# Optimization experiments

Hardware: AMD Instinct MI355X
Metric: run time of the kernel (lower is better)

Reference implementation:

```python
import jax, jax.numpy as jnp
import numpy as np

B, N_PTS, N_IN = 1, 29696, 1024
E1, E2, E3, NZ = 512, 512, 2048, 32
D1, D2, D3 = 2048, 512, 512
K = 100
V_DOF = 1.0      # Student-t dof `v`
C_CONST = 1.0    # args.c
EPS = 1e-5


def setup_inputs() -> dict:
    key = jax.random.key(0)
    ks = jax.random.split(key, 24)

    def lin_w(k, din, dout):
        return (jax.random.normal(k, (din, dout), jnp.float32) / np.float32(np.sqrt(din)))

    return {
        "x": jax.random.normal(ks[0], (B, N_PTS, N_IN), jnp.float32),
        "t1_coordinate": jax.random.normal(ks[1], (B, N_PTS, 3), jnp.float32),
        "cluster_layer": jax.random.normal(ks[2], (B, K, NZ), jnp.float32),
        "We1": lin_w(ks[3], N_IN, E1), "be1": jnp.zeros((E1,), jnp.float32),
        "We2": lin_w(ks[4], E1, E2),   "be2": jnp.zeros((E2,), jnp.float32),
        "We3": lin_w(ks[5], E2, E3),   "be3": jnp.zeros((E3,), jnp.float32),
        "Wz":  lin_w(ks[6], E3, NZ),   "bz":  jnp.zeros((NZ,), jnp.float32),
        "Wd1": lin_w(ks[7], NZ, D1),   "bd1": jnp.zeros((D1,), jnp.float32),
        "Wd2": lin_w(ks[8], D1, D2),   "bd2": jnp.zeros((D2,), jnp.float32),
        "Wd3": lin_w(ks[9], D2, D3),   "bd3": jnp.zeros((D3,), jnp.float32),
        "Wxb": lin_w(ks[10], D3, N_IN), "bxb": jnp.zeros((N_IN,), jnp.float32),
    }


def _std(a, axis=-1, keepdims=True):
    # torch.std default is unbiased (ddof=1)
    return jnp.std(a, axis=axis, keepdims=keepdims, ddof=1)


def reference(x, t1_coordinate, cluster_layer,
              We1, be1, We2, be2, We3, be3, Wz, bz,
              Wd1, bd1, Wd2, bd2, Wd3, bd3, Wxb, bxb):
    relu = jax.nn.relu
    # --- AE encode / decode ---
    h = relu(x @ We1 + be1)
    h = relu(h @ We2 + be2)
    h = relu(h @ We3 + be3)
    z = h @ Wz + bz                                   # [B, N, NZ]
    d = relu(z @ Wd1 + bd1)
    d = relu(d @ Wd2 + bd2)
    d = relu(d @ Wd3 + bd3)
    x_bar = d @ Wxb + bxb                             # [B, N, N_IN]

    # --- positional modulation + per-point normalization ---
    t1 = t1_coordinate / 100.0
    cos_mult = jnp.prod(t1, axis=-1, keepdims=True) * 0.99 + 1.0   # [B, N, 1]
    zp = z * cos_mult                                 # with_pos=True
    zp = (zp - zp.mean(axis=-1, keepdims=True)) / _std(zp)

    # --- distance to cluster centers + (inverted) Student-t assignment ---
    # [B, N, K]
    dist = jnp.sum((zp[:, :, None, :] - cluster_layer[:, None, :, :]) ** 2, axis=-1)
    q = 1.0 / (EPS + dist / V_DOF)
    q = q ** (-(V_DOF + 1.0) / 2.0)
    q = q / jnp.sum(q, axis=-1, keepdims=True)
    predict = jnp.argmax(q, axis=-1)                  # [B, N] int

    # --- stat_target_distribution (batch_size == 1 path) ---
    index = q.shape[1]                                # N_PTS
    u = q.sum(axis=1, keepdims=True)                  # [B, 1, K]
    u = (u - u.mean(axis=-1, keepdims=True)) / _std(u)

    cnt = jnp.zeros((B, K), jnp.int32).at[jnp.arange(B)[:, None], predict].add(1)
    Ncnt = jnp.where(cnt > 0, cnt, 1).astype(q.dtype)  # torch.ones init for empty clusters

    temp_q = (1.0 - q) ** 2 * jnp.log(q) * index      # [B, N, K], negative
    # v_i = sum over flat(N*K) of sqrt(-N_i / temp_q) = sqrt(N_i) * S
    S = jnp.sum(jnp.sqrt(-1.0 / temp_q), axis=(1, 2))  # [B]
    v_vec = jnp.sqrt(Ncnt) * S[:, None]               # [B, K]
    v_vec = v_vec[:, None, :]                         # [B, 1, K]
    v_vec = (v_vec - v_vec.mean(axis=-1, keepdims=True)) / _std(v_vec)
    v_vec = jax.lax.stop_gradient(v_vec)              # computed under no_grad in torch

    # batch_size == 1: global min shift
    u = u - u.min() + 0.001
    v_vec = v_vec - v_vec.min() + 0.001

    f = u + v_vec + C_CONST                           # [B, 1, K]
    w1 = q ** 2 / f
    p0 = w1 / w1.sum(axis=-1, keepdims=True)
    # first step: self.p = p, then self.p = 0.1*p + 0.9*self.p.detach()
    p = 0.1 * p0 + 0.9 * jax.lax.stop_gradient(p0)

    # --- losses ---
    kl_loss = jnp.mean(p * (jnp.log(p) - jnp.log(q))) * 0.01
    re_loss = jnp.mean((x_bar - x) ** 2)
    D = jnp.sum((cluster_layer[:, :, None, :] - cluster_layer[:, None, :, :]) ** 2, axis=-1)
    mean_distance = D.sum() / (D.size - D.shape[0] * D.shape[1])
    u_loss = (1.0 / mean_distance) * 0.01
    loss = kl_loss + re_loss + u_loss
    return predict, loss
```

## Files before the change

### kernel.cpp

```cpp
#include <hip/hip_runtime.h>
#include <math.h>

#define M_PTS 29696
#define KCL 100
#define NZ_DIM 32
#define ASTR 256

typedef _Float16 h8 __attribute__((ext_vector_type(8)));
typedef _Float16 h4 __attribute__((ext_vector_type(4)));
typedef float f4 __attribute__((ext_vector_type(4)));

__device__ __forceinline__ void load_lds16(const void* g, void* l) {
    __builtin_amdgcn_global_load_lds(
        (const __attribute__((address_space(1))) void*)g,
        (__attribute__((address_space(3))) void*)l, 16, 0, 0);
}

struct PrepW {
    const float* W[8];
    _Float16* Th[8];
    _Float16* Tl[8];
    int K[8];
    int N[8];
    int off[9];
};

__global__ __launch_bounds__(256)
void prep_weights(PrepW a, float* __restrict__ Zf, float* __restrict__ US,
                  int* __restrict__ CS, int* __restrict__ CTRS,
                  double* __restrict__ DBL)
{
    __shared__ float t[32][33];
    const int bid = blockIdx.x;
    const int tid = threadIdx.x;

    if (bid < (M_PTS*NZ_DIM/4/256)) {
        const size_t zi = ((size_t)bid*256 + tid)*4;
        *(float4*)(Zf + zi) = make_float4(0.0f, 0.0f, 0.0f, 0.0f);
    }
    if (bid == 0) {
        if (tid < KCL) { US[tid*ASTR] = 0.0f; CS[tid*ASTR] = 0; }
        if (tid == KCL) { CTRS[0] = 0; CTRS[1] = 0; }
        if (tid < 8) DBL[tid] = 0.0;
    }

    int w = 0;
    #pragma unroll
    for (int i = 1; i < 8; ++i) w += (bid >= a.off[i]);
    const int local = bid - a.off[w];
    const int K = a.K[w], N = a.N[w];
    const int tx = N >> 5;
    const int sh = __builtin_ctz(tx);
    const int n0 = (local & (tx - 1)) * 32, k0 = (local >> sh) * 32;
    const float* W = a.W[w];
    _Float16* WTh = a.Th[w];
    _Float16* WTl = a.Tl[w];

    {
        int r = tid / 8, c = (tid % 8) * 4;
        const float4 v = *(const float4*)(W + (size_t)(k0 + r) * N + n0 + c);
        t[r][c+0] = v.x; t[r][c+1] = v.y; t[r][c+2] = v.z; t[r][c+3] = v.w;
    }
    __syncthreads();
    {
        int r = tid / 8, c = (tid % 8) * 4;
        h4 hi, lo;
        #pragma unroll
        for (int u = 0; u < 4; ++u) {
            float f = t[c+u][r];
            _Float16 h = (_Float16)f;
            hi[u] = h; lo[u] = (_Float16)(f - (float)h);
        }
        *(h4*)(WTh + (size_t)(n0 + r) * K + k0 + c) = hi;
        *(h4*)(WTl + (size_t)(n0 + r) * K + k0 + c) = lo;
    }
}

template<int WM,int WN,int TM,int TN,bool RELU,int MODE,int TERMS,int ASRC=0>
__global__ __launch_bounds__(WM*WN*64)
void gemm_sp(const _Float16* __restrict__ Ahp, const _Float16* __restrict__ Alp,
             const _Float16* __restrict__ Bhp, const _Float16* __restrict__ Blp,
             const float* __restrict__ bias,
             _Float16* __restrict__ Ch, _Float16* __restrict__ Cl,
             float* __restrict__ Cf, const float* __restrict__ Xref,
             double* __restrict__ loss_acc,
             int M, int N, int K)
{
    constexpr int BM = WM*TM*16, BN = WN*TN*16, NW = WM*WN;
    constexpr int PL = (TERMS == 3) ? 2 : 1;
    constexpr int CA = BM/16, CB = BN/16;
    constexpr int STRIDE = PL*(BM+BN)*32;
    constexpr int NPW = ((MODE == 5) ? 1 : (CA/NW)*PL)
                      + ((CB >= NW) ? (CB/NW) : 1)*PL;
    constexpr int NPW_B = ((CB >= NW) ? (CB/NW) : 1)*PL;
    static_assert(ASRC == 0 || (TERMS == 3 && (CA/NW) == 2 && MODE == 0),
                  "ASRC=1 path sized for the L1 config");
    constexpr int EXTRA = (MODE == 5) ? (2048 + 4096) : 0;
    __shared__ __align__(16) _Float16 smem[2*STRIDE + EXTRA];

    const int tid = threadIdx.x;
    const int wave = tid >> 6, lane = tid & 63;
    const int wm = wave / WN, wn = wave % WN;
    const int lrow = lane & 15, lq = lane >> 4;
    const int sw = (lrow >> 1) & 3;
    const int lr4 = lane >> 2, lc4 = lane & 3;
    const int bm0 = blockIdx.y * BM, bn0 = blockIdx.x * BN;

    f4 acc[TM][TN];
    #pragma unroll
    for (int i = 0; i < TM; ++i)
        #pragma unroll
        for (int j = 0; j < TN; ++j)
            acc[i][j] = (f4)0.0f;

    auto stage = [&](int s, int k0) {
        _Float16* base = smem + s*STRIDE;
        if constexpr (MODE == 5) {
            int r_in = lane >> 2;
            int gk = (lane & 3) ^ ((r_in >> 1) & 3);
            load_lds16(Alp + (size_t)(k0 + wn*16 + r_in)*32 + gk*8,
                       smem + 2*STRIDE + s*1024 + wn*512);
        } else if constexpr (ASRC == 1) {
        } else {
            #pragma unroll
            for (int c = wave; c < CA; c += NW) {
                int r = c*16 + lr4;
                int g = lc4 ^ ((r >> 1) & 3);
                size_t goff = (size_t)(bm0 + r)*K + k0 + g*8;
                load_lds16(Ahp + goff, base + c*512);
                if (PL == 2) load_lds16(Alp + goff, base + BM*32 + c*512);
            }
        }
        if (CB >= NW) {
            #pragma unroll
            for (int c = wave; c < CB; c += NW) {
                int r = c*16 + lr4;
                int g = lc4 ^ ((r >> 1) & 3);
                size_t goff = (size_t)(bn0 + r)*K + k0 + g*8;
                load_lds16(Bhp + goff, base + PL*BM*32 + c*512);
                if (PL == 2) load_lds16(Blp + goff, base + PL*BM*32 + BN*32 + c*512);
            }
        } else {
            int c = wave % CB;
            int r = c*16 + lr4;
            int g = lc4 ^ ((r >> 1) & 3);
            size_t goff = (size_t)(bn0 + r)*K + k0 + g*8;
            load_lds16(Bhp + goff, base + PL*BM*32 + c*512);
            if (PL == 2) load_lds16(Blp + goff, base + PL*BM*32 + BN*32 + c*512);
        }
    };

    auto stageA_load = [&](int k0, float4 (&ar)[4]) {
        if constexpr (ASRC == 1) {
            #pragma unroll
            for (int u = 0; u < 2; ++u) {
                int c = wave + u*NW;
                int r = c*16 + lr4;
                int g = lc4 ^ ((r >> 1) & 3);
                const float* src = Xref + (size_t)(bm0 + r)*K + k0 + g*8;
                ar[u*2+0] = *(const float4*)(src);
                ar[u*2+1] = *(const float4*)(src + 4);
            }
        }
    };
    auto stageA_write = [&](int s, const float4 (&ar)[4]) {
        if constexpr (ASRC == 1) {
            _Float16* base = smem + s*STRIDE;
            #pragma unroll
            for (int u = 0; u < 2; ++u) {
                int c = wave + u*NW;
                float fv[8] = {ar[u*2].x, ar[u*2].y, ar[u*2].z, ar[u*2].w,
                               ar[u*2+1].x, ar[u*2+1].y, ar[u*2+1].z, ar[u*2+1].w};
                h8 hi, lo;
                #pragma unroll
                for (int q = 0; q < 8; ++q) {
                    _Float16 h = (_Float16)fv[q];
                    hi[q] = h; lo[q] = (_Float16)(fv[q] - (float)h);
                }
                *(h8*)(base + c*512 + lane*8) = hi;
                *(h8*)(base + BM*32 + c*512 + lane*8) = lo;
            }
        }
    };

    h8 zfr[(MODE == 5) ? TM : 1];
    auto computeA = [&](int ds, int s) {
        if constexpr (MODE == 5) {
            const _Float16* wslot = smem + 2*STRIDE + ds*1024 + wn*512;
            const float* bds = (const float*)(smem + 2*STRIDE + 2048);
            h8 wf = *(const h8*)(wslot + lrow*32 + ((lq ^ sw)*8));
            float bv = bds[s*32 + wn*16 + lrow];
            _Float16* areg = smem + ds*STRIDE;
            const int kc = wn*16 + lrow;
            #pragma unroll
            for (int i2 = 0; i2 < TM; ++i2) {
                f4 cc = __builtin_amdgcn_mfma_f32_16x16x32_f16(zfr[i2], wf, (f4)0.0f, 0, 0, 0);
                int cch = wm*TM + i2;
                #pragma unroll
                for (int r = 0; r < 4; ++r) {
                    float v = fmaxf(cc[r] + bv, 0.0f);
                    int r16 = lq*4 + r;
                    areg[cch*512 + r16*32 + (((kc >> 3) ^ ((r16 >> 1) & 3))*8) + (kc & 7)]
                        = (_Float16)v;
                }
            }
        }
    };

    float4 ar0[4];
    if constexpr (ASRC == 1) stageA_load(0, ar0);
    if constexpr (MODE == 5) {
        #pragma unroll
        for (int c = wave; c < 8; c += NW)
            load_lds16(Xref + c*256 + lane*4, smem + 2*STRIDE + 2048 + c*512);
        const float* zf32 = (const float*)Ahp;
        const float* bz32 = (const float*)Cl;
        float4 b0 = *(const float4*)(bz32 + lq*8);
        float4 b1 = *(const float4*)(bz32 + lq*8 + 4);
        float bb[8] = {b0.x,b0.y,b0.z,b0.w,b1.x,b1.y,b1.z,b1.w};
        #pragma unroll
        for (int i2 = 0; i2 < TM; ++i2) {
            const float* zsrc = zf32 + (size_t)(bm0 + (wm*TM + i2)*16 + lrow)*32 + lq*8;
            float4 z0 = *(const float4*)(zsrc);
            float4 z1 = *(const float4*)(zsrc + 4);
            float zz[8] = {z0.x,z0.y,z0.z,z0.w,z1.x,z1.y,z1.z,z1.w};
            #pragma unroll
            for (int q = 0; q < 8; ++q) zfr[i2][q] = (_Float16)(zz[q] + bb[q]);
        }
    }
    stage(0, 0);
    if constexpr (ASRC == 1) {
        __builtin_amdgcn_s_waitcnt(0x0F70 | NPW_B);
        stageA_write(0, ar0);
        asm volatile("s_waitcnt lgkmcnt(0)" ::: "memory");
    }
    if constexpr (MODE == 5) {
        __builtin_amdgcn_s_waitcnt(0x0F70);
        __builtin_amdgcn_s_barrier();
        computeA(0, 0);
        asm volatile("s_waitcnt lgkmcnt(0)" ::: "memory");
        __builtin_amdgcn_s_barrier();
    }

    const int steps = K >> 5;
    for (int i = 0; i < steps; ++i) {
        const int sel = i & 1;
        float4 arn[4];
        if (i + 1 < steps) {
            if constexpr (ASRC == 1) stageA_load((i + 1) << 5, arn);
            stage(sel ^ 1, (i + 1) << 5);
            __builtin_amdgcn_s_waitcnt(0x0F70 | NPW);
        } else {
            __builtin_amdgcn_s_waitcnt(0x0F70);
        }
        __builtin_amdgcn_s_barrier();

        const _Float16* base = smem + sel*STRIDE;
        h8 ah[TM], al[TM], bh[TN], bl[TN];
        #pragma unroll
        for (int i2 = 0; i2 < TM; ++i2) {
            int row = (wm*TM + i2)*16 + lrow;
            int off = row*32 + ((lq ^ sw)*8);
            ah[i2] = *(const h8*)(base + off);
            if (PL == 2) al[i2] = *(const h8*)(base + BM*32 + off);
        }
        #pragma unroll
        for (int j = 0; j < TN; ++j) {
            int row = (wn*TN + j)*16 + lrow;
            int off = row*32 + ((lq ^ sw)*8);
            bh[j] = *(const h8*)(base + PL*BM*32 + off);
            if (PL == 2) bl[j] = *(const h8*)(base + PL*BM*32 + BN*32 + off);
        }
        if constexpr (ASRC == 1) {
            if (i + 1 < steps) {
                __builtin_amdgcn_s_waitcnt(0x0F70 | NPW_B);
                stageA_write(sel ^ 1, arn);
            }
        }
        if constexpr (MODE == 5) {
            if (i + 1 < steps) {
                __builtin_amdgcn_s_waitcnt(0x0F70 | (NPW - 1));
                computeA(sel ^ 1, i + 1);
            }
        }
        #pragma unroll
        for (int i2 = 0; i2 < TM; ++i2)
            #pragma unroll
            for (int j = 0; j < TN; ++j)
                acc[i2][j] = __builtin_amdgcn_mfma_f32_16x16x32_f16(ah[i2], bh[j], acc[i2][j], 0, 0, 0);
        if (TERMS == 3) {
            #pragma unroll
            for (int i2 = 0; i2 < TM; ++i2)
                #pragma unroll
                for (int j = 0; j < TN; ++j)
                    acc[i2][j] = __builtin_amdgcn_mfma_f32_16x16x32_f16(ah[i2], bl[j], acc[i2][j], 0, 0, 0);
            #pragma unroll
            for (int i2 = 0; i2 < TM; ++i2)
                #pragma unroll
                for (int j = 0; j < TN; ++j)
                    acc[i2][j] = __builtin_amdgcn_mfma_f32_16x16x32_f16(al[i2], bh[j], acc[i2][j], 0, 0, 0);
        }
        if constexpr (MODE == 5 || ASRC == 1) {
            asm volatile("s_waitcnt lgkmcnt(0)" ::: "memory");
        }
        __builtin_amdgcn_s_barrier();
    }

    if constexpr (MODE == 4) {
        static_assert(WN*16 == 32, "MODE 4 needs N2=32 across WN waves");
        static_assert(BM*BN <= STRIDE, "MODE 4 tile planes must fit smem");
        constexpr int PLANE = BM*BN;
        constexpr int NC2 = BN/32;
        constexpr int MF2 = TM;
        const _Float16* Wh = (const _Float16*)Ch;
        const _Float16* Wl = (const _Float16*)Cl;
        _Float16* th = smem;
        _Float16* tl = smem + PLANE;

        const int n2 = wn*16 + lrow;
        h8 b2h[NC2], b2l[NC2];
        #pragma unroll
        for (int cc = 0; cc < NC2; ++cc) {
            size_t go = (size_t)n2*N + bn0 + cc*32 + lq*8;
            b2h[cc] = *(const h8*)(Wh + go);
            b2l[cc] = *(const h8*)(Wl + go);
        }

        #pragma unroll
        for (int j = 0; j < TN; ++j) {
            int col = (wn*TN + j)*16 + lrow;
            float bj = bias[bn0 + col];
            int c = col >> 5, kk = col & 31;
            #pragma unroll
            for (int i = 0; i < TM; ++i) {
                int m0 = (wm*TM + i)*16 + lq*4;
                #pragma unroll
                for (int r = 0; r < 4; ++r) {
                    float v = acc[i][j][r] + bj;
                    if (RELU) v = fmaxf(v, 0.0f);
                    int m = m0 + r;
                    int a = c*(BM*32) + m*32 + (((kk >> 3) ^ ((m >> 1) & 3))*8) + (kk & 7);
                    _Float16 hh = (_Float16)v;
                    th[a] = hh;
                    tl[a] = (_Float16)(v - (float)hh);
                }
            }
        }
        __syncthreads();

        f4 acc2[MF2];
        #pragma unroll
        for (int mf = 0; mf < MF2; ++mf) acc2[mf] = (f4)0.0f;
        #pragma unroll
        for (int mf = 0; mf < MF2; ++mf) {
            int mrow = (wm*TM + mf)*16 + lrow;
            #pragma unroll
            for (int cc = 0; cc < NC2; ++cc) {
                int off = cc*(BM*32) + mrow*32 + ((lq ^ sw)*8);
                h8 a2h = *(const h8*)(th + off);
                h8 a2l = *(const h8*)(tl + off);
                acc2[mf] = __builtin_amdgcn_mfma_f32_16x16x32_f16(a2h, b2h[cc], acc2[mf], 0, 0, 0);
                acc2[mf] = __builtin_amdgcn_mfma_f32_16x16x32_f16(a2h, b2l[cc], acc2[mf], 0, 0, 0);
                acc2[mf] = __builtin_amdgcn_mfma_f32_16x16x32_f16(a2l, b2h[cc], acc2[mf], 0, 0, 0);
            }
        }
        #pragma unroll
        for (int mf = 0; mf < MF2; ++mf) {
            int rb = bm0 + (wm*TM + mf)*16 + lq*4;
            #pragma unroll
            for (int r = 0; r < 4; ++r)
                atomicAdd(&Cf[(size_t)(rb + r)*32 + n2], acc2[mf][r]);
        }
        return;
    }

    float lsum = 0.0f;
    #pragma unroll
    for (int j = 0; j < TN; ++j) {
        int col = bn0 + (wn*TN + j)*16 + lrow;
        float bj = bias[col];
        #pragma unroll
        for (int i = 0; i < TM; ++i) {
            int rbase = bm0 + (wm*TM + i)*16 + lq*4;
            #pragma unroll
            for (int r = 0; r < 4; ++r) {
                float v = acc[i][j][r] + bj;
                if (RELU) v = fmaxf(v, 0.0f);
                size_t idx = (size_t)(rbase + r)*N + col;
                if (MODE == 2) {
                    float d = v - Xref[idx];
                    lsum = fmaf(d, d, lsum);
                } else if (MODE == 0) {
                    _Float16 hh = (_Float16)v;
                    __builtin_nontemporal_store(hh, &Ch[idx]);
                    __builtin_nontemporal_store((_Float16)(v - (float)hh), &Cl[idx]);
                } else if (MODE == 1) {
                    _Float16 hh = (_Float16)v;
                    __builtin_nontemporal_store(hh, &Ch[idx]);
                    __builtin_nontemporal_store(v, &Cf[idx]);
                } else {
                    __builtin_nontemporal_store((_Float16)v, &Ch[idx]);
                }
            }
        }
    }
    if (MODE == 2) {
        for (int off = 32; off > 0; off >>= 1) lsum += __shfl_down(lsum, off, 64);
        __syncthreads();
        float* sc = (float*)smem;
        if (lane == 0) sc[wave] = lsum;
        __syncthreads();
        if (tid == 0) {
            double t = 0.0;
            for (int w = 0; w < NW; ++w) t += (double)sc[w];
            atomicAdd(loss_acc, t);
        }
    }
}

__device__ __forceinline__ float blk_sum_f(float v, float* sh) {
    int tid = threadIdx.x;
    sh[tid] = v; __syncthreads();
    for (int s = 128; s > 0; s >>= 1) { if (tid < s) sh[tid] += sh[tid+s]; __syncthreads(); }
    float r = sh[0]; __syncthreads();
    return r;
}
__device__ __forceinline__ float blk_min_f(float v, float* sh) {
    int tid = threadIdx.x;
    sh[tid] = v; __syncthreads();
    for (int s = 128; s > 0; s >>= 1) { if (tid < s) sh[tid] = fminf(sh[tid], sh[tid+s]); __syncthreads(); }
    float r = sh[0]; __syncthreads();
    return r;
}

__global__ __launch_bounds__(256)
void cluster_pass(const float* __restrict__ z, const float* __restrict__ bz,
                  const float* __restrict__ t1,
                  const float* __restrict__ clusters,
                  float* __restrict__ D, float* __restrict__ ROWSUM,
                  float* __restrict__ pred_out, float* __restrict__ u_acc,
                  int* __restrict__ cnt, double* __restrict__ dbl,
                  float* __restrict__ f_out, int* __restrict__ blkctr)
{
    __shared__ __align__(16) float cl[KCL*33];
    __shared__ __align__(16) float Ds[64*KCL];
    __shared__ float u_s[KCL];
    __shared__ int cnt_s[KCL];
    __shared__ float swave[4];
    __shared__ float bzs[NZ_DIM];
    __shared__ int lastFlag;
    const int tid = threadIdx.x;
    const int lane = tid & 63;
    for (int i = tid; i < KCL*NZ_DIM; i += 256) cl[(i >> 5)*33 + (i & 31)] = clusters[i];
    if (tid < KCL) { u_s[tid] = 0.0f; cnt_s[tid] = 0; }
    if (tid < NZ_DIM) bzs[tid] = bz[tid];
    __syncthreads();

    const int p  = (blockIdx.x*256 + tid) >> 2;
    const int pl = tid >> 2;
    const int kg = tid & 3;

    float zr[NZ_DIM];
    const float a = t1[p*3+0]*0.01f, b = t1[p*3+1]*0.01f, c = t1[p*3+2]*0.01f;
    const float cm = a*b*c*0.99f + 1.0f;
    float mean = 0.0f;
    {
        const float4* zv = (const float4*)(z + (size_t)p*NZ_DIM);
        #pragma unroll
        for (int u = 0; u < 8; ++u) {
            float4 v = zv[u];
            zr[u*4+0] = (v.x + bzs[u*4+0])*cm; mean += zr[u*4+0];
            zr[u*4+1] = (v.y + bzs[u*4+1])*cm; mean += zr[u*4+1];
            zr[u*4+2] = (v.z + bzs[u*4+2])*cm; mean += zr[u*4+2];
            zr[u*4+3] = (v.w + bzs[u*4+3])*cm; mean += zr[u*4+3];
        }
    }
    mean *= (1.0f/NZ_DIM);
    float var = 0.0f;
    #pragma unroll
    for (int i = 0; i < NZ_DIM; ++i) { float d = zr[i]-mean; var += d*d; }
    const float istd = 1.0f / sqrtf(var * (1.0f/(NZ_DIM-1)));
    #pragma unroll
    for (int i = 0; i < NZ_DIM; ++i) zr[i] = (zr[i]-mean)*istd;

    float vals[25];
    float rowsum = 0.0f, best = -1.0f; int bk = 0;
    #pragma unroll
    for (int j = 0; j < 25; ++j) {
        const int k = kg + 4*j;
        float d = 0.0f;
        #pragma unroll
        for (int i = 0; i < NZ_DIM; ++i) { float t = zr[i]-cl[k*33+i]; d = fmaf(t,t,d); }
        float val = 1e-5f + d;
        vals[j] = val;
        rowsum += val;
        if (val > best) { best = val; bk = k; }
        Ds[pl*KCL + k] = val;
    }
    rowsum += __shfl_xor(rowsum, 1);
    rowsum += __shfl_xor(rowsum, 2);
    #pragma unroll
    for (int m = 1; m <= 2; m <<= 1) {
        float ov = __shfl_xor(best, m);
        int   ok = __shfl_xor(bk, m);
        if (ov > best || (ov == best && ok < bk)) { best = ov; bk = ok; }
    }
    if (kg == 0) {
        pred_out[p] = (float)bk;
        atomicAdd(&cnt_s[bk], 1);
        ROWSUM[p] = rowsum;
    }

    __syncthreads();
    {
        float4* dst = (float4*)(D + (size_t)blockIdx.x * (64*KCL));
        const float4* src = (const float4*)Ds;
        for (int q = tid; q < (64*KCL)/4; q += 256) dst[q] = src[q];
    }

    const float inv_rs = 1.0f/rowsum;
    float Sp = 0.0f;
    #pragma unroll
    for (int j = 0; j < 25; ++j) {
        float qv = vals[j]*inv_rs;
        float lq = logf(qv);
        float om = 1.0f - qv;
        Sp += sqrtf(-1.0f/(om*om*lq*(float)M_PTS));
        float qs = qv;
        qs += __shfl_xor(qs, 4);
        qs += __shfl_xor(qs, 8);
        qs += __shfl_xor(qs, 16);
        qs += __shfl_xor(qs, 32);
        if (lane < 4) atomicAdd(&u_s[lane + 4*j], qs);
    }
    for (int off = 32; off > 0; off >>= 1) Sp += __shfl_down(Sp, off, 64);
    if (lane == 0) swave[tid >> 6] = Sp;
    __syncthreads();
    if (tid < KCL) {
        atomicAdd(&u_acc[tid*ASTR], u_s[tid]);
        int c2 = cnt_s[tid];
        if (c2) atomicAdd(&cnt[tid*ASTR], c2);
    }
    if (tid == 0) atomicAdd(&dbl[0], (double)(swave[0]+swave[1]+swave[2]+swave[3]));

    __syncthreads();
    if (tid == 0) {
        int old = atomicAdd(blkctr, 1);
        lastFlag = (old == (int)gridDim.x - 1);
    }
    __syncthreads();
    if (!lastFlag) return;

    float* shF = cl;
    double* shD = (double*)&cl[1024];
    const bool act = (tid < KCL);
    const float S = (float)atomicAdd(&dbl[0], 0.0);

    float uv = act ? atomicAdd(&u_acc[tid*ASTR], 0.0f) : 0.0f;
    float um = blk_sum_f(uv, shF) * (1.0f/KCL);
    float ud = act ? (uv - um) : 0.0f;
    float uvar = blk_sum_f(ud*ud, shF) * (1.0f/(KCL-1));
    float un = ud / sqrtf(uvar);
    float umin = blk_min_f(act ? un : 3.0e38f, shF);
    float ufin = un - umin + 0.001f;

    float vv = 0.0f;
    if (act) { int cc2 = atomicAdd(&cnt[tid*ASTR], 0); if (cc2 < 1) cc2 = 1; vv = sqrtf((float)cc2) * S; }
    float vm = blk_sum_f(vv, shF) * (1.0f/KCL);
    float vd = act ? (vv - vm) : 0.0f;
    float vvar = blk_sum_f(vd*vd, shF) * (1.0f/(KCL-1));
    float vn = vd / sqrtf(vvar);
    float vmin = blk_min_f(act ? vn : 3.0e38f, shF);
    float vfin = vn - vmin + 0.001f;

    if (act) f_out[tid] = ufin + vfin + 1.0f;

    double dp = 0.0;
    for (int pair = tid; pair < KCL*KCL; pair += 256) {
        int i = pair / KCL, j = pair % KCL;
        float d = 0.0f;
        #pragma unroll
        for (int t2 = 0; t2 < NZ_DIM; ++t2) {
            float x = clusters[i*NZ_DIM+t2] - clusters[j*NZ_DIM+t2];
            d = fmaf(x, x, d);
        }
        dp += (double)d;
    }
    shD[tid] = dp; __syncthreads();
    for (int s = 128; s > 0; s >>= 1) { if (tid < s) shD[tid] += shD[tid+s]; __syncthreads(); }
    if (tid == 0) {
        dbl[3] = 0.01 * (double)(KCL*KCL - KCL) / shD[0];
    }
}

__global__ __launch_bounds__(256)
void kl_pass(const float* __restrict__ D, const float* __restrict__ ROWSUM,
             const float* __restrict__ f, double* __restrict__ dbl,
             float* __restrict__ out, int* __restrict__ blkctr)
{
    __shared__ __align__(16) float Ds[64*KCL];
    __shared__ float fs[KCL], lfs[KCL];
    __shared__ float swave[4];
    __shared__ int lastFlag;
    const int tid = threadIdx.x;
    const int lane = tid & 63;
    {
        const float4* src = (const float4*)(D + (size_t)blockIdx.x * (64*KCL));
        float4* dst = (float4*)Ds;
        for (int q = tid; q < (64*KCL)/4; q += 256) dst[q] = src[q];
    }
    if (tid < KCL) { float fv = f[tid]; fs[tid] = fv; lfs[tid] = logf(fv); }
    __syncthreads();

    const int p  = (blockIdx.x*256 + tid) >> 2;
    const int pl = tid >> 2;
    const int kg = tid & 3;

    float vals[25];
    #pragma unroll
    for (int j = 0; j < 25; ++j) vals[j] = Ds[pl*KCL + kg + 4*j];

    float sv = 0.0f;
    #pragma unroll
    for (int j = 0; j < 25; ++j) { float v = vals[j]; sv += v*v/fs[kg + 4*j]; }
    sv += __shfl_xor(sv, 1);
    sv += __shfl_xor(sv, 2);

    const float rowsum = ROWSUM[p];
    const float lrs = logf(rowsum), lsv = logf(sv);
    const float inv_sv = 1.0f/sv;
    float klp = 0.0f;
    #pragma unroll
    for (int j = 0; j < 25; ++j) {
        const int k = kg + 4*j;
        float v = vals[j];
        float pv = v*v/fs[k]*inv_sv;
        klp += pv*(logf(v) - lfs[k] - lsv + lrs);
    }
    for (int off = 32; off > 0; off >>= 1) klp += __shfl_down(klp, off, 64);
    if (lane == 0) swave[tid >> 6] = klp;
    __syncthreads();
    if (tid == 0) atomicAdd(&dbl[1], (double)(swave[0]+swave[1]+swave[2]+swave[3]));

    __syncthreads();
    if (tid == 0) {
        int old = atomicAdd(blkctr, 1);
        lastFlag = (old == (int)gridDim.x - 1);
    }
    __syncthreads();
    if (!lastFlag) return;
    if (tid == 0) {
        double kl = atomicAdd(&dbl[1], 0.0) / (double)((size_t)M_PTS*KCL) * 0.01;
        double re = dbl[2] / (double)((size_t)M_PTS*1024);
        out[0] = (float)(kl + re + dbl[3]);
    }
}

extern "C" void kernel_launch(void* const* d_in, const int* in_sizes, int n_in,
                              void* d_out, int out_size, void* d_ws, size_t ws_size,
                              hipStream_t stream)
{
    const float* x   = (const float*)d_in[0];
    const float* t1c = (const float*)d_in[1];
    const float* clu = (const float*)d_in[2];
    const float* We1 = (const float*)d_in[3];  const float* be1 = (const float*)d_in[4];
    const float* We2 = (const float*)d_in[5];  const float* be2 = (const float*)d_in[6];
    const float* We3 = (const float*)d_in[7];  const float* be3 = (const float*)d_in[8];
    const float* Wz  = (const float*)d_in[9];  const float* bz  = (const float*)d_in[10];
    const float* Wd1 = (const float*)d_in[11]; const float* bd1 = (const float*)d_in[12];
    const float* Wd2 = (const float*)d_in[13]; const float* bd2 = (const float*)d_in[14];
    const float* Wd3 = (const float*)d_in[15]; const float* bd3 = (const float*)d_in[16];
    const float* Wxb = (const float*)d_in[17]; const float* bxb = (const float*)d_in[18];
    float* out = (float*)d_out;

    const size_t M = M_PTS;
    _Float16* H = (_Float16*)d_ws;
    size_t o = 0;
    _Float16* BIGh = H + o; o += M*2048;
    _Float16* BIGl = H + o; o += M*2048;
    _Float16* S1h  = H + o; o += M*512;
    _Float16* S1l  = H + o; o += M*512;
    _Float16* S2h  = H + o; o += M*512;
    _Float16* S2l  = H + o; o += M*512;
    _Float16* Zh   = H + o; o += M*32;
    _Float16* Zl   = H + o; o += M*32;
    _Float16* We1h = H + o; o += 512*1024; _Float16* We1l = H + o; o += 512*1024;
    _Float16* We2h = H + o; o += 512*512;  _Float16* We2l = H + o; o += 512*512;
    _Float16* We3h = H + o; o += 2048*512; _Float16* We3l = H + o; o += 2048*512;
    _Float16* Wzh  = H + o; o += 32*2048;  _Float16* Wzl  = H + o; o += 32*2048;
    _Float16* Wd1h = H + o; o += 2048*32;  _Float16* Wd1l = H + o; o += 2048*32;
    _Float16* Wd2h = H + o; o += 512*2048; _Float16* Wd2l = H + o; o += 512*2048;
    _Float16* Wd3h = H + o; o += 512*512;  _Float16* Wd3l = H + o; o += 512*512;
    _Float16* Wxbh = H + o; o += 1024*512; _Float16* Wxbl = H + o; o += 1024*512;
    float* fpr = (float*)(H + o);
    float* Zf  = fpr;        fpr += M*32;
    float* US  = fpr;        fpr += KCL*ASTR;
    int*   CS  = (int*)fpr;  fpr += KCL*ASTR;
    float* F   = fpr;        fpr += 128;
    int*   CTRS = (int*)fpr; fpr += 16;
    double* DBL = (double*)(((uintptr_t)fpr + 15) & ~(uintptr_t)15);

    float* Dm  = (float*)S1l;
    float* RSm = (float*)S2l;

    {
        PrepW pa;
        const float* Ws[8]  = {We1, We2, We3, Wz, Wd1, Wd2, Wd3, Wxb};
        _Float16* Ths[8]    = {We1h, We2h, We3h, Wzh, Wd1h, Wd2h, Wd3h, Wxbh};
        _Float16* Tls[8]    = {We1l, We2l, We3l, Wzl, Wd1l, Wd2l, Wd3l, Wxbl};
        const int Ks[8]     = {1024, 512, 512, 2048, 32, 2048, 512, 512};
        const int Ns[8]     = {512, 512, 2048, 32, 2048, 512, 512, 1024};
        int acc = 0;
        for (int i = 0; i < 8; ++i) {
            pa.W[i] = Ws[i]; pa.Th[i] = Ths[i]; pa.Tl[i] = Tls[i];
            pa.K[i] = Ks[i]; pa.N[i] = Ns[i];
            pa.off[i] = acc;
            acc += (Ns[i] >> 5) * (Ks[i] >> 5);
        }
        pa.off[8] = acc;
        prep_weights<<<acc, 256, 0, stream>>>(pa, Zf, US, CS, CTRS, DBL);
    }

    const int MB = M_PTS/128;
    gemm_sp<2,2,4,4,true ,0,3,1><<<dim3(4,  MB), 256, 0, stream>>>(nullptr, nullptr, We1h, We1l, be1, S1h, S1l, nullptr, x, nullptr, M, 512,  1024);
    gemm_sp<2,2,4,4,true ,0,3><<<dim3(4,  MB), 256, 0, stream>>>(S1h, S1l, We2h, We2l, be2, S2h, S2l, nullptr, nullptr, nullptr, M, 512,  512);
    gemm_sp<2,2,4,4,true ,4,3><<<dim3(16, MB), 256, 0, stream>>>(S2h, S2l, We3h, We3l, be3, Wzh, Wzl, Zf, nullptr, nullptr, M, 2048, 512);
    gemm_sp<2,2,4,4,true ,5,1><<<dim3(4,  MB), 256, 0, stream>>>((const _Float16*)Zf, Wd1h, Wd2h, nullptr, bd2, S1h, (_Float16*)bz, nullptr, bd1, nullptr, M, 512,  2048);
    gemm_sp<2,2,4,4,true ,3,1><<<dim3(4,  MB), 256, 0, stream>>>(S1h, nullptr, Wd3h, nullptr, bd3, S2h,  nullptr, nullptr, nullptr, nullptr, M, 512,  512);
    gemm_sp<2,2,4,4,false,2,1><<<dim3(8,  MB), 256, 0, stream>>>(S2h, nullptr, Wxbh, nullptr, bxb, nullptr, nullptr, nullptr, x, DBL+2, M, 1024, 512);

    const int PB = (M_PTS*4)/256;
    cluster_pass<<<PB, 256, 0, stream>>>(Zf, bz, t1c, clu, Dm, RSm, out, US, CS, DBL, F, &CTRS[0]);
    kl_pass<<<PB, 256, 0, stream>>>(Dm, RSm, F, DBL, out + M_PTS, &CTRS[1]);
}
```

Baseline: 937.1 us.

## Fuse cluster and KL passes with grid-wide spin barrier, keep distances in registers

Merges the cluster-assignment and KL-loss kernels into one launch. Each block keeps its per-point distances and row sums in registers instead of writing them to global memory and reading them back. Blocks wait on a global atomic counter, then every block recomputes the small per-cluster f vector itself. The cluster-center pairwise distance term moves to block 0 before the barrier. This saves a kernel launch and a global round trip of the distance matrix. In exchange, all blocks must be co-resident: 464 blocks of 256 threads must fit on the device at once or the spin barrier deadlocks, and every block now repeats the f normalization.

New measurement: 956.9 us. 2.1% more time.

```diff
diff --git a/kernel.cpp b/kernel.cpp
--- a/kernel.cpp
+++ b/kernel.cpp
@@ -434,20 +434,22 @@
 }
 
 __global__ __launch_bounds__(256)
-void cluster_pass(const float* __restrict__ z, const float* __restrict__ bz,
-                  const float* __restrict__ t1,
-                  const float* __restrict__ clusters,
-                  float* __restrict__ D, float* __restrict__ ROWSUM,
-                  float* __restrict__ pred_out, float* __restrict__ u_acc,
-                  int* __restrict__ cnt, double* __restrict__ dbl,
-                  float* __restrict__ f_out, int* __restrict__ blkctr)
+void cluster_kl(const float* __restrict__ z, const float* __restrict__ bz,
+                const float* __restrict__ t1,
+                const float* __restrict__ clusters,
+                float* __restrict__ pred_out, float* __restrict__ u_acc,
+                int* __restrict__ cnt, double* __restrict__ dbl,
+                int* __restrict__ joinctr, int* __restrict__ blkctr,
+                float* __restrict__ out_loss)
 {
     __shared__ __align__(16) float cl[KCL*33];
-    __shared__ __align__(16) float Ds[64*KCL];
     __shared__ float u_s[KCL];
     __shared__ int cnt_s[KCL];
     __shared__ float swave[4];
     __shared__ float bzs[NZ_DIM];
+    __shared__ float fs[KCL], lfs[KCL];
+    __shared__ float sh[256];
+    __shared__ double shd[256];
     __shared__ int lastFlag;
     const int tid = threadIdx.x;
     const int lane = tid & 63;
@@ -457,7 +459,6 @@
     __syncthreads();
 
     const int p  = (blockIdx.x*256 + tid) >> 2;
-    const int pl = tid >> 2;
     const int kg = tid & 3;
 
     float zr[NZ_DIM];
@@ -495,7 +496,6 @@
         vals[j] = val;
         rowsum += val;
         if (val > best) { best = val; bk = k; }
-        Ds[pl*KCL + k] = val;
     }
     rowsum += __shfl_xor(rowsum, 1);
     rowsum += __shfl_xor(rowsum, 2);
@@ -508,14 +508,6 @@
     if (kg == 0) {
         pred_out[p] = (float)bk;
         atomicAdd(&cnt_s[bk], 1);
-        ROWSUM[p] = rowsum;
-    }
-
-    __syncthreads();
-    {
-        float4* dst = (float4*)(D + (size_t)blockIdx.x * (64*KCL));
-        const float4* src = (const float4*)Ds;
-        for (int q = tid; q < (64*KCL)/4; q += 256) dst[q] = src[q];
     }
 
     const float inv_rs = 1.0f/rowsum;
@@ -543,82 +535,55 @@
     }
     if (tid == 0) atomicAdd(&dbl[0], (double)(swave[0]+swave[1]+swave[2]+swave[3]));
 
+    if (blockIdx.x == 0) {
+        double dp = 0.0;
+        for (int pair = tid; pair < KCL*KCL; pair += 256) {
+            int i = pair / KCL, j = pair % KCL;
+            float d = 0.0f;
+            #pragma unroll
+            for (int t2 = 0; t2 < NZ_DIM; ++t2) {
+                float x = clusters[i*NZ_DIM+t2] - clusters[j*NZ_DIM+t2];
+                d = fmaf(x, x, d);
+            }
+            dp += (double)d;
+        }
+        shd[tid] = dp; __syncthreads();
+        for (int s = 128; s > 0; s >>= 1) { if (tid < s) shd[tid] += shd[tid+s]; __syncthreads(); }
+        if (tid == 0) atomicAdd(&dbl[3], 0.01 * (double)(KCL*KCL - KCL) / shd[0]);
+    }
+
     __syncthreads();
     if (tid == 0) {
-        int old = atomicAdd(blkctr, 1);
-        lastFlag = (old == (int)gridDim.x - 1);
-    }
-    __syncthreads();
-    if (!lastFlag) return;
-
-    float* shF = cl;
-    double* shD = (double*)&cl[1024];
-    const bool act = (tid < KCL);
-    const float S = (float)atomicAdd(&dbl[0], 0.0);
-
-    float uv = act ? atomicAdd(&u_acc[tid*ASTR], 0.0f) : 0.0f;
-    float um = blk_sum_f(uv, shF) * (1.0f/KCL);
-    float ud = act ? (uv - um) : 0.0f;
-    float uvar = blk_sum_f(ud*ud, shF) * (1.0f/(KCL-1));
-    float un = ud / sqrtf(uvar);
-    float umin = blk_min_f(act ? un : 3.0e38f, shF);
-    float ufin = un - umin + 0.001f;
-
-    float vv = 0.0f;
-    if (act) { int cc2 = atomicAdd(&cnt[tid*ASTR], 0); if (cc2 < 1) cc2 = 1; vv = sqrtf((float)cc2) * S; }
-    float vm = blk_sum_f(vv, shF) * (1.0f/KCL);
-    float vd = act ? (vv - vm) : 0.0f;
-    float vvar = blk_sum_f(vd*vd, shF) * (1.0f/(KCL-1));
-    float vn = vd / sqrtf(vvar);
-    float vmin = blk_min_f(act ? vn : 3.0e38f, shF);
-    float vfin = vn - vmin + 0.001f;
-
-    if (act) f_out[tid] = ufin + vfin + 1.0f;
-
-    double dp = 0.0;
-    for (int pair = tid; pair < KCL*KCL; pair += 256) {
-        int i = pair / KCL, j = pair % KCL;
-        float d = 0.0f;
-        #pragma unroll
-        for (int t2 = 0; t2 < NZ_DIM; ++t2) {
-            float x = clusters[i*NZ_DIM+t2] - clusters[j*NZ_DIM+t2];
-            d = fmaf(x, x, d);
-        }
-        dp += (double)d;
-    }
-    shD[tid] = dp; __syncthreads();
-    for (int s = 128; s > 0; s >>= 1) { if (tid < s) shD[tid] += shD[tid+s]; __syncthreads(); }
-    if (tid == 0) {
-        dbl[3] = 0.01 * (double)(KCL*KCL - KCL) / shD[0];
-    }
-}
-
-__global__ __launch_bounds__(256)
-void kl_pass(const float* __restrict__ D, const float* __restrict__ ROWSUM,
-             const float* __restrict__ f, double* __restrict__ dbl,
-             float* __restrict__ out, int* __restrict__ blkctr)
-{
-    __shared__ __align__(16) float Ds[64*KCL];
-    __shared__ float fs[KCL], lfs[KCL];
-    __shared__ float swave[4];
-    __shared__ int lastFlag;
-    const int tid = threadIdx.x;
-    const int lane = tid & 63;
+        atomicAdd(joinctr, 1);
+        while (atomicAdd(joinctr, 0) < (int)gridDim.x)
+            __builtin_amdgcn_s_sleep(16);
+    }
+    __syncthreads();
+
     {
-        const float4* src = (const float4*)(D + (size_t)blockIdx.x * (64*KCL));
-        float4* dst = (float4*)Ds;
-        for (int q = tid; q < (64*KCL)/4; q += 256) dst[q] = src[q];
-    }
-    if (tid < KCL) { float fv = f[tid]; fs[tid] = fv; lfs[tid] = logf(fv); }
-    __syncthreads();
-
-    const int p  = (blockIdx.x*256 + tid) >> 2;
-    const int pl = tid >> 2;
-    const int kg = tid & 3;
-
-    float vals[25];
-    #pragma unroll
-    for (int j = 0; j < 25; ++j) vals[j] = Ds[pl*KCL + kg + 4*j];
+        const bool act = (tid < KCL);
+        const float S = (float)atomicAdd(&dbl[0], 0.0);
+
+        float uv = act ? atomicAdd(&u_acc[tid*ASTR], 0.0f) : 0.0f;
+        float um = blk_sum_f(uv, sh) * (1.0f/KCL);
+        float ud = act ? (uv - um) : 0.0f;
+        float uvar = blk_sum_f(ud*ud, sh) * (1.0f/(KCL-1));
+        float un = ud / sqrtf(uvar);
+        float umin = blk_min_f(act ? un : 3.0e38f, sh);
+        float ufin = un - umin + 0.001f;
+
+        float vv = 0.0f;
+        if (act) { int cc2 = atomicAdd(&cnt[tid*ASTR], 0); if (cc2 < 1) cc2 = 1; vv = sqrtf((float)cc2) * S; }
+        float vm = blk_sum_f(vv, sh) * (1.0f/KCL);
+        float vd = act ? (vv - vm) : 0.0f;
+        float vvar = blk_sum_f(vd*vd, sh) * (1.0f/(KCL-1));
+        float vn = vd / sqrtf(vvar);
+        float vmin = blk_min_f(act ? vn : 3.0e38f, sh);
+        float vfin = vn - vmin + 0.001f;
+
+        if (act) { float fv = ufin + vfin + 1.0f; fs[tid] = fv; lfs[tid] = logf(fv); }
+    }
+    __syncthreads();
 
     float sv = 0.0f;
     #pragma unroll
@@ -626,7 +591,6 @@
     sv += __shfl_xor(sv, 1);
     sv += __shfl_xor(sv, 2);
 
-    const float rowsum = ROWSUM[p];
     const float lrs = logf(rowsum), lsv = logf(sv);
     const float inv_sv = 1.0f/sv;
     float klp = 0.0f;
@@ -652,7 +616,8 @@
     if (tid == 0) {
         double kl = atomicAdd(&dbl[1], 0.0) / (double)((size_t)M_PTS*KCL) * 0.01;
         double re = dbl[2] / (double)((size_t)M_PTS*1024);
-        out[0] = (float)(kl + re + dbl[3]);
+        double ul = atomicAdd(&dbl[3], 0.0);
+        out_loss[0] = (float)(kl + re + ul);
     }
 }
 
@@ -700,9 +665,6 @@
     int*   CTRS = (int*)fpr; fpr += 16;
     double* DBL = (double*)(((uintptr_t)fpr + 15) & ~(uintptr_t)15);
 
-    float* Dm  = (float*)S1l;
-    float* RSm = (float*)S2l;
-
     {
         PrepW pa;
         const float* Ws[8]  = {We1, We2, We3, Wz, Wd1, Wd2, Wd3, Wxb};
@@ -730,6 +692,6 @@
     gemm_sp<2,2,4,4,false,2,1><<<dim3(8,  MB), 256, 0, stream>>>(S2h, nullptr, Wxbh, nullptr, bxb, nullptr, nullptr, nullptr, x, DBL+2, M, 1024, 512);
 
     const int PB = (M_PTS*4)/256;
-    cluster_pass<<<PB, 256, 0, stream>>>(Zf, bz, t1c, clu, Dm, RSm, out, US, CS, DBL, F, &CTRS[0]);
-    kl_pass<<<PB, 256, 0, stream>>>(Dm, RSm, F, DBL, out + M_PTS, &CTRS[1]);
+    cluster_kl<<<PB, 256, 0, stream>>>(Zf, bz, t1c, clu, out, US, CS, DBL,
+                                       &CTRS[0], &CTRS[1], out + M_PTS);
 }
```
